# Kernel optimization log

Measured on AMD Instinct MI355X. Metric: run time of the kernel, lower is better.

Reference implementation:

```python
import jax, jax.numpy as jnp
import numpy as np

N, D = 96, 512
EPS = 1e-8
INV_TEMP = 100.0  # 1 / 0.01


def _pair_indices(n):
    # all ordered pairs (i, j) with i != j, row-major like the original loops
    i, j = np.meshgrid(np.arange(n), np.arange(n), indexing='ij')
    mask = i != j
    return jnp.asarray(i[mask]), jnp.asarray(j[mask])


def setup_inputs() -> dict:
    key = jax.random.key(0)
    k1, k2 = jax.random.split(key)
    return {
        "txtf": jax.random.normal(k1, (N, D), dtype=jnp.float32),
        "imgf": jax.random.normal(k2, (N, D), dtype=jnp.float32),
    }


def reference(txtf, imgf):
    n = txtf.shape[0]
    ii, jj = _pair_indices(n)  # [P], P = n*(n-1)

    td = txtf[ii] - txtf[jj]                                   # [P, D]
    td = td / (jnp.linalg.norm(td, axis=-1, keepdims=True) + EPS)
    im = imgf[ii] - imgf[jj]                                   # [P, D]
    im = im / (jnp.linalg.norm(im, axis=-1, keepdims=True) + EPS)

    mma = jnp.einsum('pd,qd->pq', td, im) * INV_TEMP           # [P, P]
    diag = jnp.arange(mma.shape[0])
    # CE(mma, labels): softmax over rows; CE(mma.T, labels): softmax over cols
    lp_row = jax.nn.log_softmax(mma, axis=-1)
    lp_col = jax.nn.log_softmax(mma, axis=0)
    loss1 = -jnp.mean(lp_row[diag, diag])
    loss2 = -jnp.mean(lp_col[diag, diag])
    return (loss1 + loss2) * 0.5
```

## Files before the change

kernel.cpp:

```cpp
#include <hip/hip_runtime.h>
#include <math.h>

#define NN 96
#define DD 512
#define PP 9120
#define EPSF 1e-8f
#define INV_TEMP 100.0f
#define LOG2E 1.4426950408889634f
#define RT 8
#define NTASK (2*PP)
#define NBLK_T (NTASK/RT)
#define CBASE (PP/RT)
#define NPBLK 1152

#define OFF_G     0
#define OFF_GT    9216
#define OFF_WT    18432
#define OFF_WM    27648
#define OFF_WST   36864
#define OFF_WSM   46080
#define OFF_WMAXS 55296

__device__ __forceinline__ void decomp(unsigned p, int& i, int& j) {
    unsigned ii = p / 95u;
    unsigned r  = p - ii * 95u;
    i = (int)ii;
    j = (int)(r + (r >= ii ? 1u : 0u));
}

__global__ __launch_bounds__(256) void prep_kernel(const float* __restrict__ txt,
                                                   const float* __restrict__ img,
                                                   float* __restrict__ ws) {
    __shared__ float wtw[4], wmw[4];
    int b = blockIdx.x, tid = threadIdx.x;
    int lane = tid & 63, wv = tid >> 6;
    const float4* T4 = (const float4*)txt;
    const float4* M4 = (const float4*)img;
    float bwt = 0.f, bwm = 0.f;

    #pragma unroll
    for (int q = 0; q < 2; ++q) {
        int pp = b * 8 + wv * 2 + q;
        int i = pp / NN, j = pp - i * NN;
        const float4* Ti = T4 + i * 128 + 2 * lane;
        const float4* Tj = T4 + j * 128 + 2 * lane;
        const float4* Mi = M4 + i * 128 + 2 * lane;
        const float4* Mj = M4 + j * 128 + 2 * lane;
        float gij = 0.f, nt2 = 0.f, nm2 = 0.f;
        #pragma unroll
        for (int u = 0; u < 2; ++u) {
            float4 a = Ti[u], t = Tj[u], c = Mi[u], d = Mj[u];
            gij += a.x*d.x + a.y*d.y + a.z*d.z + a.w*d.w;
            float d0 = a.x-t.x, d1 = a.y-t.y, d2 = a.z-t.z, d3 = a.w-t.w;
            nt2 += d0*d0 + d1*d1 + d2*d2 + d3*d3;
            float e0 = c.x-d.x, e1 = c.y-d.y, e2 = c.z-d.z, e3 = c.w-d.w;
            nm2 += e0*e0 + e1*e1 + e2*e2 + e3*e3;
        }
        #pragma unroll
        for (int off = 32; off > 0; off >>= 1) {
            gij += __shfl_xor(gij, off, 64);
            nt2 += __shfl_xor(nt2, off, 64);
            nm2 += __shfl_xor(nm2, off, 64);
        }
        float wt = 0.f, wm = 0.f;
        if (i != j) {
            wt = 1.f / (sqrtf(fmaxf(nt2, 0.f)) + EPSF);
            wm = 1.f / (sqrtf(fmaxf(nm2, 0.f)) + EPSF);
        }
        bwt = fmaxf(bwt, wt); bwm = fmaxf(bwm, wm);
        if (lane == 0) {
            int t0 = i * NN + j;
            ws[OFF_G  + t0] = gij;
            ws[OFF_GT + j * NN + i] = gij;
            ws[OFF_WT  + t0] = wt;
            ws[OFF_WM  + t0] = wm;
            ws[OFF_WST + t0] = wt * LOG2E;
            ws[OFF_WSM + t0] = wm * LOG2E;
        }
    }
    if (lane == 0) { wtw[wv] = bwt; wmw[wv] = bwm; }
    __syncthreads();
    if (tid == 0) {
        ws[OFF_WMAXS + b]         = fmaxf(fmaxf(wtw[0], wtw[1]), fmaxf(wtw[2], wtw[3]));
        ws[OFF_WMAXS + NPBLK + b] = fmaxf(fmaxf(wmw[0], wmw[1]), fmaxf(wmw[2], wmw[3]));
    }
}

__global__ __launch_bounds__(256) void lse_kernel(const float* __restrict__ ws,
                                                  float* __restrict__ out) {
    __shared__ float A[RT * NN];
    __shared__ float M2s[RT];
    __shared__ float Ms[RT];
    __shared__ float wred[4][RT];
    __shared__ float cred[RT];

    int tid = threadIdx.x, lane = tid & 63, wv = tid >> 6;
    int b = blockIdx.x;
    bool is_col = (b >= CBASE);
    const float* Mat    = ws + (is_col ? OFF_GT  : OFF_G);
    const float* wself  = ws + (is_col ? OFF_WM  : OFF_WT);
    const float* wsweep = ws + (is_col ? OFF_WST : OFF_WSM);

    const float* wmx = ws + OFF_WMAXS + (is_col ? 0 : NPBLK);
    float wl = 0.f;
    #pragma unroll
    for (int u = 0; u < 18; ++u)
        wl = fmaxf(wl, wmx[lane + 64 * u]);
    #pragma unroll
    for (int off = 32; off > 0; off >>= 1)
        wl = fmaxf(wl, __shfl_xor(wl, off, 64));
    float Wmax = wl;
    int base = (b - (is_col ? CBASE : 0)) * RT;

    #pragma unroll
    for (int q = 0; q < 2; ++q) {
        int rr = 2 * wv + q;
        int i, j; decomp((unsigned)(base + rr), i, j);
        float s = INV_TEMP * wself[i * NN + j];
        const float* Mi = Mat + i * NN;
        const float* Mj = Mat + j * NN;
        float v0 = s * (Mi[lane] - Mj[lane]);
        A[rr * NN + lane] = v0;
        float vmax = v0, vmin = v0;
        if (lane < 32) {
            float v1 = s * (Mi[64 + lane] - Mj[64 + lane]);
            A[rr * NN + 64 + lane] = v1;
            vmax = fmaxf(vmax, v1); vmin = fminf(vmin, v1);
        }
        #pragma unroll
        for (int off = 32; off > 0; off >>= 1) {
            vmax = fmaxf(vmax, __shfl_xor(vmax, off, 64));
            vmin = fminf(vmin, __shfl_xor(vmin, off, 64));
        }
        if (lane == 0) {
            float M = Wmax * (vmax - vmin);
            Ms[rr] = M;
            M2s[rr] = M * LOG2E;
        }
    }
    __syncthreads();

    int l1 = (lane < 32) ? (64 + lane) : (lane - 32);
    float M2[RT], aL0[RT], aL1[RT], aL2[RT], S[RT];
    #pragma unroll
    for (int r = 0; r < RT; ++r) {
        M2[r] = M2s[r];
        aL0[r] = A[r * NN + lane];
        aL1[r] = A[r * NN + l1];
        aL2[r] = A[r * NN + lane + 32];
        S[r] = 0.f;
    }

    {
        int k0n = 2 * wv;
        float nw0 = wsweep[k0n * NN + lane];
        float nw1 = wsweep[(lane < 32 ? k0n : k0n + 1) * NN + l1];
        float nw2 = wsweep[(k0n + 1) * NN + lane + 32];
        for (int u = 0; u < 12; ++u) {
            int k0 = 2 * (wv + 4 * u);
            float w0 = nw0, w1 = nw1, w2 = nw2;
            if (u < 11) {
                int nk0 = 2 * (wv + 4 * (u + 1));
                nw0 = wsweep[nk0 * NN + lane];
                nw1 = wsweep[(lane < 32 ? nk0 : nk0 + 1) * NN + l1];
                nw2 = wsweep[(nk0 + 1) * NN + lane + 32];
            }
            #pragma unroll
            for (int r = 0; r < RT; ++r) {
                float2 ak = *(const float2*)&A[r * NN + k0];
                float aksel = (lane < 32) ? ak.x : ak.y;
                S[r] += __builtin_amdgcn_exp2f(w0 * (ak.x  - aL0[r]) - M2[r])
                      + __builtin_amdgcn_exp2f(w1 * (aksel - aL1[r]) - M2[r])
                      + __builtin_amdgcn_exp2f(w2 * (ak.y  - aL2[r]) - M2[r]);
            }
        }
    }

    #pragma unroll
    for (int off = 32; off > 0; off >>= 1) {
        #pragma unroll
        for (int r = 0; r < RT; ++r) S[r] += __shfl_xor(S[r], off, 64);
    }
    if (lane == 0) {
        #pragma unroll
        for (int r = 0; r < RT; ++r) wred[wv][r] = S[r];
    }
    __syncthreads();

    if (tid < RT) {
        int r = tid;
        float tot = wred[0][r] + wred[1][r] + wred[2][r] + wred[3][r];
        tot -= 96.f * __builtin_amdgcn_exp2f(-M2s[r]);
        int i, j; decomp((unsigned)(base + r), i, j);
        float wtv = ws[OFF_WT + i * NN + j];
        float wmv = ws[OFF_WM + i * NN + j];
        float gii = ws[OFF_G + i * NN + i], gjj = ws[OFF_G + j * NN + j];
        float gij = ws[OFF_G + i * NN + j], gji = ws[OFF_G + j * NN + i];
        float dia = INV_TEMP * wtv * wmv * (gii - gij - gji + gjj);
        cred[r] = Ms[r] + logf(tot) - dia;
    }
    __syncthreads();
    if (tid == 0) {
        float c = 0.f;
        #pragma unroll
        for (int r = 0; r < RT; ++r) c += cred[r];
        atomicAdd(out, c * (1.0f / (float)NTASK));
    }
}

extern "C" void kernel_launch(void* const* d_in, const int* in_sizes, int n_in,
                              void* d_out, int out_size, void* d_ws, size_t ws_size,
                              hipStream_t stream) {
    const float* txt = (const float*)d_in[0];
    const float* img = (const float*)d_in[1];
    float* ws = (float*)d_ws;
    prep_kernel<<<NPBLK, 256, 0, stream>>>(txt, img, ws);
    lse_kernel<<<NBLK_T, 256, 0, stream>>>(ws, (float*)d_out);
}
```

Baseline: 96.38 us.

## Make each wavefront own its rows in the LSE sweep, removing block syncs

The LSE kernel changes from 8 rows per 256-thread block, with the k-sweep split across 4 wavefronts, to 4 rows per wavefront, each wavefront sweeping all 96 k values alone, two wavefronts per block. This removes the __syncthreads barriers and the shared-memory cross-wave reduction, and each wave issues its own atomic. The cost is twice as many wsweep loads per row, since each weight load now serves 4 rows instead of 8, and twice as many atomics.

```diff
diff --git a/kernel.cpp b/kernel.cpp
--- a/kernel.cpp
+++ b/kernel.cpp
@@ -7,10 +7,10 @@
 #define EPSF 1e-8f
 #define INV_TEMP 100.0f
 #define LOG2E 1.4426950408889634f
-#define RT 8
+#define RTW 4
+#define WPB 2
 #define NTASK (2*PP)
-#define NBLK_T (NTASK/RT)
-#define CBASE (PP/RT)
+#define LBLK (NTASK/(RTW*WPB))
 #define NPBLK 1152
 
 #define OFF_G     0
@@ -86,20 +86,19 @@
     }
 }
 
-__global__ __launch_bounds__(256) void lse_kernel(const float* __restrict__ ws,
+__global__ __launch_bounds__(128) void lse_kernel(const float* __restrict__ ws,
                                                   float* __restrict__ out) {
-    __shared__ float A[RT * NN];
-    __shared__ float M2s[RT];
-    __shared__ float Ms[RT];
-    __shared__ float wred[4][RT];
-    __shared__ float cred[RT];
+    __shared__ float A[WPB][RTW][NN];
 
     int tid = threadIdx.x, lane = tid & 63, wv = tid >> 6;
     int b = blockIdx.x;
-    bool is_col = (b >= CBASE);
+    int tw = (b * WPB + wv) * RTW;
+    bool is_col = (tw >= PP);
+    int base = tw - (is_col ? PP : 0);
     const float* Mat    = ws + (is_col ? OFF_GT  : OFF_G);
     const float* wself  = ws + (is_col ? OFF_WM  : OFF_WT);
     const float* wsweep = ws + (is_col ? OFF_WST : OFF_WSM);
+    float (*Aw)[NN] = A[wv];
 
     const float* wmx = ws + OFF_WMAXS + (is_col ? 0 : NPBLK);
     float wl = 0.f;
@@ -110,21 +109,21 @@
     for (int off = 32; off > 0; off >>= 1)
         wl = fmaxf(wl, __shfl_xor(wl, off, 64));
     float Wmax = wl;
-    int base = (b - (is_col ? CBASE : 0)) * RT;
 
+    float aL0[RTW], M2[RTW];
     #pragma unroll
-    for (int q = 0; q < 2; ++q) {
-        int rr = 2 * wv + q;
-        int i, j; decomp((unsigned)(base + rr), i, j);
+    for (int r = 0; r < RTW; ++r) {
+        int i, j; decomp((unsigned)(base + r), i, j);
         float s = INV_TEMP * wself[i * NN + j];
         const float* Mi = Mat + i * NN;
         const float* Mj = Mat + j * NN;
         float v0 = s * (Mi[lane] - Mj[lane]);
-        A[rr * NN + lane] = v0;
+        Aw[r][lane] = v0;
+        aL0[r] = v0;
         float vmax = v0, vmin = v0;
         if (lane < 32) {
             float v1 = s * (Mi[64 + lane] - Mj[64 + lane]);
-            A[rr * NN + 64 + lane] = v1;
+            Aw[r][64 + lane] = v1;
             vmax = fmaxf(vmax, v1); vmin = fminf(vmin, v1);
         }
         #pragma unroll
@@ -132,79 +131,60 @@
             vmax = fmaxf(vmax, __shfl_xor(vmax, off, 64));
             vmin = fminf(vmin, __shfl_xor(vmin, off, 64));
         }
-        if (lane == 0) {
-            float M = Wmax * (vmax - vmin);
-            Ms[rr] = M;
-            M2s[rr] = M * LOG2E;
-        }
+        M2[r] = Wmax * (vmax - vmin) * LOG2E;
     }
-    __syncthreads();
 
     int l1 = (lane < 32) ? (64 + lane) : (lane - 32);
-    float M2[RT], aL0[RT], aL1[RT], aL2[RT], S[RT];
+    float aL1[RTW], aL2[RTW], S[RTW];
     #pragma unroll
-    for (int r = 0; r < RT; ++r) {
-        M2[r] = M2s[r];
-        aL0[r] = A[r * NN + lane];
-        aL1[r] = A[r * NN + l1];
-        aL2[r] = A[r * NN + lane + 32];
+    for (int r = 0; r < RTW; ++r) {
+        aL1[r] = Aw[r][l1];
+        aL2[r] = Aw[r][lane + 32];
         S[r] = 0.f;
     }
 
-    {
-        int k0n = 2 * wv;
-        float nw0 = wsweep[k0n * NN + lane];
-        float nw1 = wsweep[(lane < 32 ? k0n : k0n + 1) * NN + l1];
-        float nw2 = wsweep[(k0n + 1) * NN + lane + 32];
-        for (int u = 0; u < 12; ++u) {
-            int k0 = 2 * (wv + 4 * u);
-            float w0 = nw0, w1 = nw1, w2 = nw2;
-            if (u < 11) {
-                int nk0 = 2 * (wv + 4 * (u + 1));
-                nw0 = wsweep[nk0 * NN + lane];
-                nw1 = wsweep[(lane < 32 ? nk0 : nk0 + 1) * NN + l1];
-                nw2 = wsweep[(nk0 + 1) * NN + lane + 32];
-            }
-            #pragma unroll
-            for (int r = 0; r < RT; ++r) {
-                float2 ak = *(const float2*)&A[r * NN + k0];
-                float aksel = (lane < 32) ? ak.x : ak.y;
-                S[r] += __builtin_amdgcn_exp2f(w0 * (ak.x  - aL0[r]) - M2[r])
-                      + __builtin_amdgcn_exp2f(w1 * (aksel - aL1[r]) - M2[r])
-                      + __builtin_amdgcn_exp2f(w2 * (ak.y  - aL2[r]) - M2[r]);
-            }
+    #pragma unroll 4
+    for (int u = 0; u < 48; ++u) {
+        int k0 = 2 * u, k1 = k0 + 1;
+        float w0 = wsweep[k0 * NN + lane];
+        float w1 = wsweep[(lane < 32 ? k0 : k1) * NN + l1];
+        float w2 = wsweep[k1 * NN + lane + 32];
+        #pragma unroll
+        for (int r = 0; r < RTW; ++r) {
+            float2 ak = *(const float2*)&Aw[r][k0];
+            float aksel = (lane < 32) ? ak.x : ak.y;
+            S[r] += __builtin_amdgcn_exp2f(w0 * (ak.x  - aL0[r]) - M2[r])
+                  + __builtin_amdgcn_exp2f(w1 * (aksel - aL1[r]) - M2[r])
+                  + __builtin_amdgcn_exp2f(w2 * (ak.y  - aL2[r]) - M2[r]);
         }
     }
 
     #pragma unroll
     for (int off = 32; off > 0; off >>= 1) {
         #pragma unroll
-        for (int r = 0; r < RT; ++r) S[r] += __shfl_xor(S[r], off, 64);
+        for (int r = 0; r < RTW; ++r) S[r] += __shfl_xor(S[r], off, 64);
     }
-    if (lane == 0) {
-        #pragma unroll
-        for (int r = 0; r < RT; ++r) wred[wv][r] = S[r];
-    }
-    __syncthreads();
 
-    if (tid < RT) {
-        int r = tid;
-        float tot = wred[0][r] + wred[1][r] + wred[2][r] + wred[3][r];
-        tot -= 96.f * __builtin_amdgcn_exp2f(-M2s[r]);
-        int i, j; decomp((unsigned)(base + r), i, j);
+    if (lane < RTW) {
+        float tot = S[0], M2sel = M2[0];
+        tot   = (lane == 1) ? S[1]  : tot;
+        tot   = (lane == 2) ? S[2]  : tot;
+        tot   = (lane == 3) ? S[3]  : tot;
+        M2sel = (lane == 1) ? M2[1] : M2sel;
+        M2sel = (lane == 2) ? M2[2] : M2sel;
+        M2sel = (lane == 3) ? M2[3] : M2sel;
+        tot -= 96.f * __builtin_amdgcn_exp2f(-M2sel);
+        int i, j; decomp((unsigned)(base + lane), i, j);
         float wtv = ws[OFF_WT + i * NN + j];
         float wmv = ws[OFF_WM + i * NN + j];
         float gii = ws[OFF_G + i * NN + i], gjj = ws[OFF_G + j * NN + j];
         float gij = ws[OFF_G + i * NN + j], gji = ws[OFF_G + j * NN + i];
         float dia = INV_TEMP * wtv * wmv * (gii - gij - gji + gjj);
-        cred[r] = Ms[r] + logf(tot) - dia;
-    }
-    __syncthreads();
-    if (tid == 0) {
-        float c = 0.f;
-        #pragma unroll
-        for (int r = 0; r < RT; ++r) c += cred[r];
-        atomicAdd(out, c * (1.0f / (float)NTASK));
+        float c = M2sel * (1.0f / LOG2E) + logf(tot) - dia;
+        c += __shfl_xor(c, 1, 64);
+        c += __shfl_xor(c, 2, 64);
+        if (lane == 0)
+            atomicAdd(out, c * (1.0f / (float)NTASK));
     }
 }
 
@@ -215,5 +195,5 @@
     const float* img = (const float*)d_in[1];
     float* ws = (float*)d_ws;
     prep_kernel<<<NPBLK, 256, 0, stream>>>(txt, img, ws);
-    lse_kernel<<<NBLK_T, 256, 0, stream>>>(ws, (float*)d_out);
+    lse_kernel<<<LBLK, 128, 0, stream>>>(ws, (float*)d_out);
 }
```

Measured after the change: 131.7 us. 1.37x slower.
